# Kernel tuning notes

Measured on AMD Instinct MI355X. Metric: run time of the kernel, lower is better.

Reference implementation:

```python
import jax, jax.numpy as jnp
import numpy as np

NDET = 16
N_UP = 8  # spin_split=2 with nelec=16 -> (8, 8)


def _orbitals(s, r, W, b, pi, a):
    """FermiNet orbital layer for one spin.

    s: (B, n, d) backflow stream, r: (B, n, nion, 3) electron-ion displacements,
    W: (d, n*NDET), b: (n*NDET,), pi/a: (nion, n*NDET).
    Returns (NDET, B, n, n) square orbital matrices.
    """
    lin = s @ W + b                                   # (B, n, n*NDET)
    dist = jnp.linalg.norm(r, axis=-1)                # (B, n, nion)
    # isotropic envelope: sum_ion pi[ion, orb] * exp(-a[ion, orb] * |r - R_ion|)
    env = jnp.sum(pi * jnp.exp(-a * dist[..., None]), axis=-2)  # (B, n, n*NDET)
    orb = lin * env
    n = orb.shape[-2]
    orb = orb.reshape(*orb.shape[:-1], NDET, n)       # (B, n, NDET, n)
    return jnp.moveaxis(orb, -2, 0)                   # (NDET, B, n, n)


def setup_inputs() -> dict:
    key = jax.random.key(0)
    ks = jax.random.split(key, 10)
    B, NE, D, NION = 4096, 16, 256, 4
    no = N_UP * NDET
    sc = 1.0 / np.sqrt(D)
    return {
        "stream_1e": jax.random.normal(ks[0], (B, NE, D), jnp.float32),
        "r_ei": jax.random.normal(ks[1], (B, NE, NION, 3), jnp.float32),
        "W_up": jax.random.normal(ks[2], (D, no), jnp.float32) * sc,
        "b_up": jax.random.normal(ks[3], (no,), jnp.float32) * 0.01,
        "pi_up": jax.random.normal(ks[4], (NION, no), jnp.float32),
        "a_up": jax.random.uniform(ks[5], (NION, no), jnp.float32, 0.5, 1.5),
        "W_dn": jax.random.normal(ks[6], (D, no), jnp.float32) * sc,
        "b_dn": jax.random.normal(ks[7], (no,), jnp.float32) * 0.01,
        "pi_dn": jax.random.normal(ks[8], (NION, no), jnp.float32),
        "a_dn": jax.random.uniform(ks[9], (NION, no), jnp.float32, 0.5, 1.5),
    }


def reference(stream_1e, r_ei, W_up, b_up, pi_up, a_up, W_dn, b_dn, pi_dn, a_dn):
    s_up, s_dn = stream_1e[:, :N_UP], stream_1e[:, N_UP:]
    r_up, r_dn = r_ei[:, :N_UP], r_ei[:, N_UP:]
    orb_u = _orbitals(s_up, r_up, W_up, b_up, pi_up, a_up)  # (NDET, B, 8, 8)
    orb_d = _orbitals(s_dn, r_dn, W_dn, b_dn, pi_dn, a_dn)
    sgn_u, log_u = jnp.linalg.slogdet(orb_u)                # (NDET, B)
    sgn_d, log_d = jnp.linalg.slogdet(orb_d)
    sign = sgn_u * sgn_d
    logd = log_u + log_d
    # psi = sum_i det_u_i * det_d_i  (PARALLEL_EVEN, determinant_fn=None)
    m = jnp.max(logd, axis=0)                               # (B,)
    ssum = jnp.sum(sign * jnp.exp(logd - m), axis=0)        # (B,)
    log_psi = m + jnp.log(jnp.abs(ssum))                    # (B,)
    return log_psi
```

## Files before the change

kernel.cpp:

```cpp
#include <hip/hip_runtime.h>
#include <math.h>

#define DD 256
#define NO 128
#define WT_PLANE 65536
#define ORW 132
#define ORB_WAVE (32*ORW)
#define UNI_US 33792
#define BUF_US 16384

typedef __attribute__((ext_vector_type(8))) short bf16x8;
typedef __attribute__((ext_vector_type(4))) float f32x4;

static __device__ inline unsigned short f2bf(float x) {
    unsigned int u = __float_as_uint(x);
    unsigned int r = (u + 0x7FFFu + ((u >> 16) & 1u)) >> 16;
    return (unsigned short)r;
}
static __device__ inline float bf2f(unsigned short h) {
    return __uint_as_float(((unsigned int)h) << 16);
}

__global__ void prep_wt(const float* __restrict__ Wu, const float* __restrict__ Wd,
                        unsigned short* __restrict__ wt) {
    const int n    = blockIdx.x & 127;
    const int spin = blockIdx.x >> 7;
    const float* W = spin ? Wd : Wu;
    const int t = threadIdx.x;
    for (int kk = t; kk < DD; kk += 64) {
        const float x = W[(size_t)kk * NO + n];
        const unsigned short h = f2bf(x);
        const unsigned short l = f2bf(x - bf2f(h));
        const size_t o = ((size_t)spin * NO + n) * DD + kk;
        wt[o]            = h;
        wt[WT_PLANE + o] = l;
    }
}

__global__ __launch_bounds__(256, 2)
void fermi_main(const float* __restrict__ stream1e, const float* __restrict__ r_ei,
                const float* __restrict__ bu, const float* __restrict__ piu,
                const float* __restrict__ au, const float* __restrict__ bd,
                const float* __restrict__ pid_, const float* __restrict__ ad,
                const unsigned short* __restrict__ wt, float* __restrict__ out)
{
    __shared__ __align__(16) unsigned short uni[UNI_US];
    __shared__ __align__(16) float distL[4 * 32 * 4];
    __shared__ float exL[2 * 8 * 16 * 2];

    float* orb = (float*)uni;

    const int t    = threadIdx.x;
    const int w    = t >> 6;
    const int lane = t & 63;
    const int lr   = lane & 15;
    const int lg   = lane >> 4;
    const int sp   = w >> 1;
    const int bh   = w & 1;
    const int b0   = blockIdx.x * 8;

    #pragma unroll
    for (int i = 0; i < 2; ++i) {
        const int idx = lane * 2 + i;
        const int row = idx >> 2, ion = idx & 3;
        const int b  = b0 + bh * 4 + (row >> 3);
        const int ge = sp * 8 + (row & 7);
        const float* rp = r_ei + (((size_t)b * 16 + ge) * 4 + ion) * 3;
        const float x = rp[0], y = rp[1], z = rp[2];
        distL[(w * 32 + row) * 4 + ion] = sqrtf(x * x + y * y + z * z);
    }

    size_t arow0, arow1;
    {
        const int r0 = lr;
        const int r1 = 16 + lr;
        arow0 = (((size_t)(b0 + bh * 4 + (r0 >> 3)) * 16) + sp * 8 + (r0 & 7)) * DD;
        arow1 = (((size_t)(b0 + bh * 4 + (r1 >> 3)) * 16) + sp * 8 + (r1 & 7)) * DD;
    }

    auto stage = [&](int buf, int kt) {
        const int k0 = kt * 32;
        #pragma unroll
        for (int i = 0; i < 8; ++i) {
            const int idx  = i * 256 + t;
            const int row  = idx >> 2;
            const int slot = idx & 3;
            const uint4 v = *(const uint4*)(wt + (size_t)(row >> 8) * WT_PLANE
                                               + (size_t)(row & 255) * DD + k0 + slot * 8);
            *(uint4*)(uni + buf * BUF_US + row * 32 + ((slot + row) & 3) * 8) = v;
        }
    };

    f32x4 acc[2][8];
    #pragma unroll
    for (int mt = 0; mt < 2; ++mt)
        #pragma unroll
        for (int nt = 0; nt < 8; ++nt)
            acc[mt][nt] = (f32x4){0.f, 0.f, 0.f, 0.f};

    stage(0, 0);
    __syncthreads();

    for (int kt = 0; kt < 8; ++kt) {
        if (kt < 7) stage((kt + 1) & 1, kt + 1);

        const int k0 = kt * 32;
        bf16x8 ah[2], al[2];
        #pragma unroll
        for (int mt = 0; mt < 2; ++mt) {
            const float* ap = stream1e + (mt ? arow1 : arow0) + k0 + lg * 8;
            const float4 v0 = *(const float4*)ap;
            const float4 v1 = *(const float4*)(ap + 4);
            const float f[8] = {v0.x, v0.y, v0.z, v0.w, v1.x, v1.y, v1.z, v1.w};
            int hw[4], lw[4];
            #pragma unroll
            for (int p = 0; p < 4; ++p) {
                unsigned int hp;
                asm("v_cvt_pk_bf16_f32 %0, %1, %2" : "=v"(hp) : "v"(f[2*p]), "v"(f[2*p+1]));
                const float h0 = __uint_as_float(hp << 16);
                const float h1 = __uint_as_float(hp & 0xFFFF0000u);
                const float l0 = f[2*p]   - h0;
                const float l1 = f[2*p+1] - h1;
                unsigned int lp;
                asm("v_cvt_pk_bf16_f32 %0, %1, %2" : "=v"(lp) : "v"(l0), "v"(l1));
                hw[p] = (int)hp;
                lw[p] = (int)lp;
            }
            ah[mt] = *(const bf16x8*)hw;
            al[mt] = *(const bf16x8*)lw;
        }

        const unsigned short* bufp = uni + (kt & 1) * BUF_US;
        const int rot = ((lg + lr) & 3) * 8;
        #pragma unroll
        for (int nt = 0; nt < 8; ++nt) {
            const int rhi = sp * 128 + nt * 16 + lr;
            const bf16x8 bh_ = *(const bf16x8*)(bufp + rhi * 32 + rot);
            const bf16x8 bl_ = *(const bf16x8*)(bufp + 8192 + rhi * 32 + rot);
            acc[0][nt] = __builtin_amdgcn_mfma_f32_16x16x32_bf16(ah[0], bh_, acc[0][nt], 0, 0, 0);
            acc[0][nt] = __builtin_amdgcn_mfma_f32_16x16x32_bf16(ah[0], bl_, acc[0][nt], 0, 0, 0);
            acc[0][nt] = __builtin_amdgcn_mfma_f32_16x16x32_bf16(al[0], bh_, acc[0][nt], 0, 0, 0);
            acc[1][nt] = __builtin_amdgcn_mfma_f32_16x16x32_bf16(ah[1], bh_, acc[1][nt], 0, 0, 0);
            acc[1][nt] = __builtin_amdgcn_mfma_f32_16x16x32_bf16(ah[1], bl_, acc[1][nt], 0, 0, 0);
            acc[1][nt] = __builtin_amdgcn_mfma_f32_16x16x32_bf16(al[1], bh_, acc[1][nt], 0, 0, 0);
        }
        __syncthreads();
    }

    const float* pi_s = sp ? pid_ : piu;
    const float* a_s  = sp ? ad   : au;
    const float* b_s  = sp ? bd   : bu;
    float* ow = orb + (size_t)w * ORB_WAVE;
    {
        float dq[2][4][4];
        #pragma unroll
        for (int mt = 0; mt < 2; ++mt)
            #pragma unroll
            for (int q = 0; q < 4; ++q) {
                const int row = mt * 16 + lg * 4 + q;
                const f32x4 dv = *(const f32x4*)&distL[(w * 32 + row) * 4];
                dq[mt][q][0] = dv[0]; dq[mt][q][1] = dv[1];
                dq[mt][q][2] = dv[2]; dq[mt][q][3] = dv[3];
            }
        #pragma unroll
        for (int nt = 0; nt < 8; ++nt) {
            const int C = nt * 16 + lr;
            float pv[4], av[4];
            #pragma unroll
            for (int ion = 0; ion < 4; ++ion) {
                pv[ion] = pi_s[ion * NO + C];
                av[ion] = a_s [ion * NO + C];
            }
            const float bias = b_s[C];
            #pragma unroll
            for (int mt = 0; mt < 2; ++mt)
                #pragma unroll
                for (int q = 0; q < 4; ++q) {
                    float env = 0.f;
                    #pragma unroll
                    for (int ion = 0; ion < 4; ++ion)
                        env += pv[ion] * __expf(-av[ion] * dq[mt][q][ion]);
                    ow[(mt * 16 + lg * 4 + q) * ORW + C] = (acc[mt][nt][q] + bias) * env;
                }
        }
    }

    {
        const int bl_ = lane >> 4;
        const int dd  = lane & 15;
        float M[8][8];
        #pragma unroll
        for (int e = 0; e < 8; ++e) {
            const float* pr = ow + (bl_ * 8 + e) * ORW + dd * 8;
            const f32x4 u0 = *(const f32x4*)pr;
            const f32x4 u1 = *(const f32x4*)(pr + 4);
            M[e][0] = u0[0]; M[e][1] = u0[1]; M[e][2] = u0[2]; M[e][3] = u0[3];
            M[e][4] = u1[0]; M[e][5] = u1[1]; M[e][6] = u1[2]; M[e][7] = u1[3];
        }
        float ldet = 0.f, sgn = 1.f;
        #pragma unroll
        for (int c = 0; c < 8; ++c) {
            #pragma unroll
            for (int r = c + 1; r < 8; ++r) {
                const bool swp = fabsf(M[r][c]) > fabsf(M[c][c]);
                sgn = swp ? -sgn : sgn;
                #pragma unroll
                for (int j = c; j < 8; ++j) {
                    const float x1 = M[c][j], x2 = M[r][j];
                    M[c][j] = swp ? x2 : x1;
                    M[r][j] = swp ? x1 : x2;
                }
            }
            const float p = M[c][c];
            ldet += __logf(fabsf(p));
            sgn  = (p < 0.f) ? -sgn : sgn;
            const float rp = (p != 0.f) ? (1.0f / p) : 0.f;
            #pragma unroll
            for (int r = c + 1; r < 8; ++r) {
                const float fm = M[r][c] * rp;
                #pragma unroll
                for (int j = c + 1; j < 8; ++j)
                    M[r][j] = fmaf(-fm, M[c][j], M[r][j]);
            }
        }
        const int bb = bh * 4 + bl_;
        exL[((sp * 8 + bb) * 16 + dd) * 2 + 0] = ldet;
        exL[((sp * 8 + bb) * 16 + dd) * 2 + 1] = sgn;
    }
    __syncthreads();

    if (t < 128) {
        const int b  = t >> 4;
        const int d2 = t & 15;
        const float lu  = exL[((b)     * 16 + d2) * 2 + 0];
        const float su  = exL[((b)     * 16 + d2) * 2 + 1];
        const float ldn = exL[((8 + b) * 16 + d2) * 2 + 0];
        const float sdn = exL[((8 + b) * 16 + d2) * 2 + 1];
        const float l   = lu + ldn;
        const float s   = su * sdn;
        float m = l;
        #pragma unroll
        for (int off = 1; off <= 8; off <<= 1) m = fmaxf(m, __shfl_xor(m, off));
        float ss = s * __expf(l - m);
        #pragma unroll
        for (int off = 1; off <= 8; off <<= 1) ss += __shfl_xor(ss, off);
        if (d2 == 0) out[b0 + b] = m + __logf(fabsf(ss));
    }
}

extern "C" void kernel_launch(void* const* d_in, const int* in_sizes, int n_in,
                              void* d_out, int out_size, void* d_ws, size_t ws_size,
                              hipStream_t stream) {
    (void)n_in; (void)in_sizes; (void)ws_size;
    const float* s1e  = (const float*)d_in[0];
    const float* r_ei = (const float*)d_in[1];
    const float* Wu   = (const float*)d_in[2];
    const float* bu   = (const float*)d_in[3];
    const float* piu  = (const float*)d_in[4];
    const float* au   = (const float*)d_in[5];
    const float* Wd   = (const float*)d_in[6];
    const float* bd   = (const float*)d_in[7];
    const float* pid_ = (const float*)d_in[8];
    const float* ad   = (const float*)d_in[9];
    float* out = (float*)d_out;
    unsigned short* wt = (unsigned short*)d_ws;

    hipLaunchKernelGGL(prep_wt, dim3(256), dim3(64), 0, stream, Wu, Wd, wt);

    const int B = out_size;
    hipLaunchKernelGGL(fermi_main, dim3(B / 8), dim3(256), 0, stream,
                       s1e, r_ei, bu, piu, au, bd, pid_, ad, wt, out);
}
```

Baseline: 36.31 us.

## Pre-swizzle weights into MFMA fragment order and read B operands directly from global

The prep kernel now writes the bf16 hi/lo weight split in the exact per-lane MFMA fragment layout, so the main kernel loads B operands straight from global/L2 with one 16-byte load per lane. This removes the LDS double-buffer staging and the per-k-tile barriers, and shrinks shared memory to just the orbital buffer. The prep kernel is also reworked for coalesced reads. The determinant stage loads rows in a lane-rotated order to spread LDS bank accesses, adjusting the starting sign for the cyclic row permutation. The risk is that every wave now re-reads weights from cache rather than sharing one LDS copy.

```diff
diff --git a/kernel.cpp b/kernel.cpp
--- a/kernel.cpp
+++ b/kernel.cpp
@@ -3,11 +3,8 @@
 
 #define DD 256
 #define NO 128
-#define WT_PLANE 65536
 #define ORW 132
 #define ORB_WAVE (32*ORW)
-#define UNI_US 33792
-#define BUF_US 16384
 
 typedef __attribute__((ext_vector_type(8))) short bf16x8;
 typedef __attribute__((ext_vector_type(4))) float f32x4;
@@ -21,20 +18,20 @@
     return __uint_as_float(((unsigned int)h) << 16);
 }
 
-__global__ void prep_wt(const float* __restrict__ Wu, const float* __restrict__ Wd,
-                        unsigned short* __restrict__ wt) {
-    const int n    = blockIdx.x & 127;
+__global__ void prep_wt2(const float* __restrict__ Wu, const float* __restrict__ Wd,
+                         unsigned short* __restrict__ wt2) {
     const int spin = blockIdx.x >> 7;
-    const float* W = spin ? Wd : Wu;
-    const int t = threadIdx.x;
-    for (int kk = t; kk < DD; kk += 64) {
-        const float x = W[(size_t)kk * NO + n];
-        const unsigned short h = f2bf(x);
-        const unsigned short l = f2bf(x - bf2f(h));
-        const size_t o = ((size_t)spin * NO + n) * DD + kk;
-        wt[o]            = h;
-        wt[WT_PLANE + o] = l;
-    }
+    const int k    = (blockIdx.x & 127) * 2 + (threadIdx.x >> 7);
+    const int n    = threadIdx.x & 127;
+    const float x  = (spin ? Wd : Wu)[(size_t)k * NO + n];
+    const unsigned short h = f2bf(x);
+    const unsigned short l = f2bf(x - bf2f(h));
+    const int kt = k >> 5, lg = (k >> 3) & 3, j = k & 7;
+    const int nt = n >> 4, lr = n & 15;
+    const size_t o = (size_t)spin * 65536 + kt * 8192 + nt * 1024
+                   + (lg * 16 + lr) * 8 + j;
+    wt2[o]       = h;
+    wt2[o + 512] = l;
 }
 
 __global__ __launch_bounds__(256, 2)
@@ -42,13 +39,11 @@
                 const float* __restrict__ bu, const float* __restrict__ piu,
                 const float* __restrict__ au, const float* __restrict__ bd,
                 const float* __restrict__ pid_, const float* __restrict__ ad,
-                const unsigned short* __restrict__ wt, float* __restrict__ out)
+                const unsigned short* __restrict__ wt2, float* __restrict__ out)
 {
-    __shared__ __align__(16) unsigned short uni[UNI_US];
+    __shared__ __align__(16) float orb[4 * ORB_WAVE];
     __shared__ __align__(16) float distL[4 * 32 * 4];
     __shared__ float exL[2 * 8 * 16 * 2];
-
-    float* orb = (float*)uni;
 
     const int t    = threadIdx.x;
     const int w    = t >> 6;
@@ -77,19 +72,7 @@
         arow0 = (((size_t)(b0 + bh * 4 + (r0 >> 3)) * 16) + sp * 8 + (r0 & 7)) * DD;
         arow1 = (((size_t)(b0 + bh * 4 + (r1 >> 3)) * 16) + sp * 8 + (r1 & 7)) * DD;
     }
-
-    auto stage = [&](int buf, int kt) {
-        const int k0 = kt * 32;
-        #pragma unroll
-        for (int i = 0; i < 8; ++i) {
-            const int idx  = i * 256 + t;
-            const int row  = idx >> 2;
-            const int slot = idx & 3;
-            const uint4 v = *(const uint4*)(wt + (size_t)(row >> 8) * WT_PLANE
-                                               + (size_t)(row & 255) * DD + k0 + slot * 8);
-            *(uint4*)(uni + buf * BUF_US + row * 32 + ((slot + row) & 3) * 8) = v;
-        }
-    };
+    const unsigned short* wb = wt2 + (size_t)sp * 65536 + lane * 8;
 
     f32x4 acc[2][8];
     #pragma unroll
@@ -98,12 +81,8 @@
         for (int nt = 0; nt < 8; ++nt)
             acc[mt][nt] = (f32x4){0.f, 0.f, 0.f, 0.f};
 
-    stage(0, 0);
-    __syncthreads();
-
+    #pragma unroll
     for (int kt = 0; kt < 8; ++kt) {
-        if (kt < 7) stage((kt + 1) & 1, kt + 1);
-
         const int k0 = kt * 32;
         bf16x8 ah[2], al[2];
         #pragma unroll
@@ -129,14 +108,11 @@
             ah[mt] = *(const bf16x8*)hw;
             al[mt] = *(const bf16x8*)lw;
         }
-
-        const unsigned short* bufp = uni + (kt & 1) * BUF_US;
-        const int rot = ((lg + lr) & 3) * 8;
         #pragma unroll
         for (int nt = 0; nt < 8; ++nt) {
-            const int rhi = sp * 128 + nt * 16 + lr;
-            const bf16x8 bh_ = *(const bf16x8*)(bufp + rhi * 32 + rot);
-            const bf16x8 bl_ = *(const bf16x8*)(bufp + 8192 + rhi * 32 + rot);
+            const unsigned short* fp_ = wb + kt * 8192 + nt * 1024;
+            const bf16x8 bh_ = *(const bf16x8*)fp_;
+            const bf16x8 bl_ = *(const bf16x8*)(fp_ + 512);
             acc[0][nt] = __builtin_amdgcn_mfma_f32_16x16x32_bf16(ah[0], bh_, acc[0][nt], 0, 0, 0);
             acc[0][nt] = __builtin_amdgcn_mfma_f32_16x16x32_bf16(ah[0], bl_, acc[0][nt], 0, 0, 0);
             acc[0][nt] = __builtin_amdgcn_mfma_f32_16x16x32_bf16(al[0], bh_, acc[0][nt], 0, 0, 0);
@@ -144,7 +120,6 @@
             acc[1][nt] = __builtin_amdgcn_mfma_f32_16x16x32_bf16(ah[1], bl_, acc[1][nt], 0, 0, 0);
             acc[1][nt] = __builtin_amdgcn_mfma_f32_16x16x32_bf16(al[1], bh_, acc[1][nt], 0, 0, 0);
         }
-        __syncthreads();
     }
 
     const float* pi_s = sp ? pid_ : piu;
@@ -188,16 +163,18 @@
     {
         const int bl_ = lane >> 4;
         const int dd  = lane & 15;
+        const int rot = (lane >> 2) & 7;
         float M[8][8];
         #pragma unroll
-        for (int e = 0; e < 8; ++e) {
+        for (int j = 0; j < 8; ++j) {
+            const int e = (j + rot) & 7;
             const float* pr = ow + (bl_ * 8 + e) * ORW + dd * 8;
             const f32x4 u0 = *(const f32x4*)pr;
             const f32x4 u1 = *(const f32x4*)(pr + 4);
-            M[e][0] = u0[0]; M[e][1] = u0[1]; M[e][2] = u0[2]; M[e][3] = u0[3];
-            M[e][4] = u1[0]; M[e][5] = u1[1]; M[e][6] = u1[2]; M[e][7] = u1[3];
-        }
-        float ldet = 0.f, sgn = 1.f;
+            M[j][0] = u0[0]; M[j][1] = u0[1]; M[j][2] = u0[2]; M[j][3] = u0[3];
+            M[j][4] = u1[0]; M[j][5] = u1[1]; M[j][6] = u1[2]; M[j][7] = u1[3];
+        }
+        float ldet = 0.f, sgn = (rot & 1) ? -1.f : 1.f;
         #pragma unroll
         for (int c = 0; c < 8; ++c) {
             #pragma unroll
@@ -263,11 +240,11 @@
     const float* pid_ = (const float*)d_in[8];
     const float* ad   = (const float*)d_in[9];
     float* out = (float*)d_out;
-    unsigned short* wt = (unsigned short*)d_ws;
-
-    hipLaunchKernelGGL(prep_wt, dim3(256), dim3(64), 0, stream, Wu, Wd, wt);
+    unsigned short* wt2 = (unsigned short*)d_ws;
+
+    hipLaunchKernelGGL(prep_wt2, dim3(256), dim3(256), 0, stream, Wu, Wd, wt2);
 
     const int B = out_size;
     hipLaunchKernelGGL(fermi_main, dim3(B / 8), dim3(256), 0, stream,
-                       s1e, r_ei, bu, piu, au, bd, pid_, ad, wt, out);
-}
+                       s1e, r_ei, bu, piu, au, bd, pid_, ad, wt2, out);
+}
```

New measurement: 42.05 us. +15.8%, slower.

## Register-prefetch weight tiles and A operands, rotate determinant row loads

Applied to the files above, without the earlier changes.

The weight-tile staging now loads the next k-slice from global memory into registers before the MFMA loop and writes it to the alternate LDS buffer only after the MFMAs, so global latency overlaps with compute. The fp32 activation rows for the next k-step are also prefetched into registers one iteration ahead. In the determinant stage, each lane loads matrix rows in a rotated order to spread LDS bank accesses, and the sign is corrected for the cyclic row permutation. This raises register pressure in exchange for hiding load latency and reducing LDS bank conflicts.

```diff
diff --git a/kernel.cpp b/kernel.cpp
--- a/kernel.cpp
+++ b/kernel.cpp
@@ -78,18 +78,8 @@
         arow1 = (((size_t)(b0 + bh * 4 + (r1 >> 3)) * 16) + sp * 8 + (r1 & 7)) * DD;
     }
 
-    auto stage = [&](int buf, int kt) {
-        const int k0 = kt * 32;
-        #pragma unroll
-        for (int i = 0; i < 8; ++i) {
-            const int idx  = i * 256 + t;
-            const int row  = idx >> 2;
-            const int slot = idx & 3;
-            const uint4 v = *(const uint4*)(wt + (size_t)(row >> 8) * WT_PLANE
-                                               + (size_t)(row & 255) * DD + k0 + slot * 8);
-            *(uint4*)(uni + buf * BUF_US + row * 32 + ((slot + row) & 3) * 8) = v;
-        }
-    };
+    const int srow_base = t >> 2;
+    const int sslot     = t & 3;
 
     f32x4 acc[2][8];
     #pragma unroll
@@ -98,20 +88,54 @@
         for (int nt = 0; nt < 8; ++nt)
             acc[mt][nt] = (f32x4){0.f, 0.f, 0.f, 0.f};
 
-    stage(0, 0);
+    uint4 sregs[8];
+    #pragma unroll
+    for (int i = 0; i < 8; ++i) {
+        const int row = srow_base + i * 64;
+        sregs[i] = *(const uint4*)(wt + (size_t)(row >> 8) * WT_PLANE
+                                      + (size_t)(row & 255) * DD + sslot * 8);
+    }
+    float4 aq[2][2];
+    #pragma unroll
+    for (int mt = 0; mt < 2; ++mt) {
+        const float* ap = stream1e + (mt ? arow1 : arow0) + lg * 8;
+        aq[mt][0] = *(const float4*)ap;
+        aq[mt][1] = *(const float4*)(ap + 4);
+    }
+    #pragma unroll
+    for (int i = 0; i < 8; ++i) {
+        const int row = srow_base + i * 64;
+        *(uint4*)(uni + row * 32 + ((sslot + row) & 3) * 8) = sregs[i];
+    }
     __syncthreads();
 
+    #pragma unroll
     for (int kt = 0; kt < 8; ++kt) {
-        if (kt < 7) stage((kt + 1) & 1, kt + 1);
-
-        const int k0 = kt * 32;
+        const int cur = kt & 1;
+        if (kt < 7) {
+            const int k0n = (kt + 1) * 32;
+            #pragma unroll
+            for (int i = 0; i < 8; ++i) {
+                const int row = srow_base + i * 64;
+                sregs[i] = *(const uint4*)(wt + (size_t)(row >> 8) * WT_PLANE
+                                              + (size_t)(row & 255) * DD + k0n + sslot * 8);
+            }
+        }
+        float4 an[2][2];
+        if (kt < 7) {
+            const int k0n = (kt + 1) * 32;
+            #pragma unroll
+            for (int mt = 0; mt < 2; ++mt) {
+                const float* ap = stream1e + (mt ? arow1 : arow0) + k0n + lg * 8;
+                an[mt][0] = *(const float4*)ap;
+                an[mt][1] = *(const float4*)(ap + 4);
+            }
+        }
         bf16x8 ah[2], al[2];
         #pragma unroll
         for (int mt = 0; mt < 2; ++mt) {
-            const float* ap = stream1e + (mt ? arow1 : arow0) + k0 + lg * 8;
-            const float4 v0 = *(const float4*)ap;
-            const float4 v1 = *(const float4*)(ap + 4);
-            const float f[8] = {v0.x, v0.y, v0.z, v0.w, v1.x, v1.y, v1.z, v1.w};
+            const float f[8] = {aq[mt][0].x, aq[mt][0].y, aq[mt][0].z, aq[mt][0].w,
+                                aq[mt][1].x, aq[mt][1].y, aq[mt][1].z, aq[mt][1].w};
             int hw[4], lw[4];
             #pragma unroll
             for (int p = 0; p < 4; ++p) {
@@ -129,8 +153,7 @@
             ah[mt] = *(const bf16x8*)hw;
             al[mt] = *(const bf16x8*)lw;
         }
-
-        const unsigned short* bufp = uni + (kt & 1) * BUF_US;
+        const unsigned short* bufp = uni + cur * BUF_US;
         const int rot = ((lg + lr) & 3) * 8;
         #pragma unroll
         for (int nt = 0; nt < 8; ++nt) {
@@ -144,7 +167,22 @@
             acc[1][nt] = __builtin_amdgcn_mfma_f32_16x16x32_bf16(ah[1], bl_, acc[1][nt], 0, 0, 0);
             acc[1][nt] = __builtin_amdgcn_mfma_f32_16x16x32_bf16(al[1], bh_, acc[1][nt], 0, 0, 0);
         }
+        if (kt < 7) {
+            unsigned short* dst = uni + (cur ^ 1) * BUF_US;
+            #pragma unroll
+            for (int i = 0; i < 8; ++i) {
+                const int row = srow_base + i * 64;
+                *(uint4*)(dst + row * 32 + ((sslot + row) & 3) * 8) = sregs[i];
+            }
+        }
         __syncthreads();
+        if (kt < 7) {
+            #pragma unroll
+            for (int mt = 0; mt < 2; ++mt) {
+                aq[mt][0] = an[mt][0];
+                aq[mt][1] = an[mt][1];
+            }
+        }
     }
 
     const float* pi_s = sp ? pid_ : piu;
@@ -188,16 +226,18 @@
     {
         const int bl_ = lane >> 4;
         const int dd  = lane & 15;
+        const int rot = (lane >> 2) & 7;
         float M[8][8];
         #pragma unroll
-        for (int e = 0; e < 8; ++e) {
+        for (int j = 0; j < 8; ++j) {
+            const int e = (j + rot) & 7;
             const float* pr = ow + (bl_ * 8 + e) * ORW + dd * 8;
             const f32x4 u0 = *(const f32x4*)pr;
             const f32x4 u1 = *(const f32x4*)(pr + 4);
-            M[e][0] = u0[0]; M[e][1] = u0[1]; M[e][2] = u0[2]; M[e][3] = u0[3];
-            M[e][4] = u1[0]; M[e][5] = u1[1]; M[e][6] = u1[2]; M[e][7] = u1[3];
-        }
-        float ldet = 0.f, sgn = 1.f;
+            M[j][0] = u0[0]; M[j][1] = u0[1]; M[j][2] = u0[2]; M[j][3] = u0[3];
+            M[j][4] = u1[0]; M[j][5] = u1[1]; M[j][6] = u1[2]; M[j][7] = u1[3];
+        }
+        float ldet = 0.f, sgn = (rot & 1) ? -1.f : 1.f;
         #pragma unroll
         for (int c = 0; c < 8; ++c) {
             #pragma unroll
```

New measurement: 39.51 us. 8.8% more time.

## Pre-swizzle weights and stage them via direct global-to-LDS loads

Applied to the files above, without the earlier changes.

The prep kernel now writes the bf16 hi/lo weight planes in the exact per-k-tile, bank-rotated order the main kernel uses in shared memory. Staging can therefore use global_load_lds 16-byte copies that bypass registers. The k loop is fully unrolled. Determinant matrix rows are loaded in a lane-dependent rotated order to spread LDS bank accesses, and the initial sign is flipped for odd rotations to compensate. The extra unrolling raises code size and register pressure, and the async copy depends on the compiler synchronizing correctly.

```diff
diff --git a/kernel.cpp b/kernel.cpp
--- a/kernel.cpp
+++ b/kernel.cpp
@@ -3,7 +3,6 @@
 
 #define DD 256
 #define NO 128
-#define WT_PLANE 65536
 #define ORW 132
 #define ORB_WAVE (32*ORW)
 #define UNI_US 33792
@@ -21,19 +20,27 @@
     return __uint_as_float(((unsigned int)h) << 16);
 }
 
-__global__ void prep_wt(const float* __restrict__ Wu, const float* __restrict__ Wd,
-                        unsigned short* __restrict__ wt) {
+static __device__ __forceinline__ void gl_lds16(const void* g, void* l) {
+    __builtin_amdgcn_global_load_lds(
+        (const __attribute__((address_space(1))) void*)g,
+        (__attribute__((address_space(3))) void*)l, 16, 0, 0);
+}
+
+__global__ void prep_wt3(const float* __restrict__ Wu, const float* __restrict__ Wd,
+                         unsigned short* __restrict__ wt3) {
     const int n    = blockIdx.x & 127;
     const int spin = blockIdx.x >> 7;
     const float* W = spin ? Wd : Wu;
     const int t = threadIdx.x;
-    for (int kk = t; kk < DD; kk += 64) {
-        const float x = W[(size_t)kk * NO + n];
+    for (int k = t; k < DD; k += 64) {
+        const float x = W[(size_t)k * NO + n];
         const unsigned short h = f2bf(x);
         const unsigned short l = f2bf(x - bf2f(h));
-        const size_t o = ((size_t)spin * NO + n) * DD + kk;
-        wt[o]            = h;
-        wt[WT_PLANE + o] = l;
+        const int kt = k >> 5, slot = (k >> 3) & 3, j = k & 7;
+        const int rh = spin * 128 + n;
+        const int rl = 256 + rh;
+        wt3[(size_t)kt * 16384 + rh * 32 + ((slot + rh) & 3) * 8 + j] = h;
+        wt3[(size_t)kt * 16384 + rl * 32 + ((slot + rl) & 3) * 8 + j] = l;
     }
 }
 
@@ -79,16 +86,11 @@
     }
 
     auto stage = [&](int buf, int kt) {
-        const int k0 = kt * 32;
-        #pragma unroll
-        for (int i = 0; i < 8; ++i) {
-            const int idx  = i * 256 + t;
-            const int row  = idx >> 2;
-            const int slot = idx & 3;
-            const uint4 v = *(const uint4*)(wt + (size_t)(row >> 8) * WT_PLANE
-                                               + (size_t)(row & 255) * DD + k0 + slot * 8);
-            *(uint4*)(uni + buf * BUF_US + row * 32 + ((slot + row) & 3) * 8) = v;
-        }
+        const unsigned short* gsrc = wt + (size_t)kt * 16384 + w * 4096 + lane * 8;
+        unsigned short* ldst = uni + buf * BUF_US + w * 4096;
+        #pragma unroll
+        for (int i = 0; i < 8; ++i)
+            gl_lds16(gsrc + i * 512, ldst + i * 512);
     };
 
     f32x4 acc[2][8];
@@ -101,8 +103,10 @@
     stage(0, 0);
     __syncthreads();
 
+    #pragma unroll
     for (int kt = 0; kt < 8; ++kt) {
-        if (kt < 7) stage((kt + 1) & 1, kt + 1);
+        const int cur = kt & 1;
+        if (kt < 7) stage(cur ^ 1, kt + 1);
 
         const int k0 = kt * 32;
         bf16x8 ah[2], al[2];
@@ -129,8 +133,7 @@
             ah[mt] = *(const bf16x8*)hw;
             al[mt] = *(const bf16x8*)lw;
         }
-
-        const unsigned short* bufp = uni + (kt & 1) * BUF_US;
+        const unsigned short* bufp = uni + cur * BUF_US;
         const int rot = ((lg + lr) & 3) * 8;
         #pragma unroll
         for (int nt = 0; nt < 8; ++nt) {
@@ -188,16 +191,18 @@
     {
         const int bl_ = lane >> 4;
         const int dd  = lane & 15;
+        const int rot = (lane >> 2) & 7;
         float M[8][8];
         #pragma unroll
-        for (int e = 0; e < 8; ++e) {
+        for (int j = 0; j < 8; ++j) {
+            const int e = (j + rot) & 7;
             const float* pr = ow + (bl_ * 8 + e) * ORW + dd * 8;
             const f32x4 u0 = *(const f32x4*)pr;
             const f32x4 u1 = *(const f32x4*)(pr + 4);
-            M[e][0] = u0[0]; M[e][1] = u0[1]; M[e][2] = u0[2]; M[e][3] = u0[3];
-            M[e][4] = u1[0]; M[e][5] = u1[1]; M[e][6] = u1[2]; M[e][7] = u1[3];
-        }
-        float ldet = 0.f, sgn = 1.f;
+            M[j][0] = u0[0]; M[j][1] = u0[1]; M[j][2] = u0[2]; M[j][3] = u0[3];
+            M[j][4] = u1[0]; M[j][5] = u1[1]; M[j][6] = u1[2]; M[j][7] = u1[3];
+        }
+        float ldet = 0.f, sgn = (rot & 1) ? -1.f : 1.f;
         #pragma unroll
         for (int c = 0; c < 8; ++c) {
             #pragma unroll
@@ -263,11 +268,11 @@
     const float* pid_ = (const float*)d_in[8];
     const float* ad   = (const float*)d_in[9];
     float* out = (float*)d_out;
-    unsigned short* wt = (unsigned short*)d_ws;
-
-    hipLaunchKernelGGL(prep_wt, dim3(256), dim3(64), 0, stream, Wu, Wd, wt);
+    unsigned short* wt3 = (unsigned short*)d_ws;
+
+    hipLaunchKernelGGL(prep_wt3, dim3(256), dim3(64), 0, stream, Wu, Wd, wt3);
 
     const int B = out_size;
     hipLaunchKernelGGL(fermi_main, dim3(B / 8), dim3(256), 0, stream,
-                       s1e, r_ei, bu, piu, au, bd, pid_, ad, wt, out);
-}
+                       s1e, r_ei, bu, piu, au, bd, pid_, ad, wt3, out);
+}
```

Result: slower. 37.09 us (+2.1%).
